# Kernel optimization log

Measured on AMD Instinct MI355X. Metric: run time of the kernel, lower is better.

The kernel has to match this reference:

```python
import jax, jax.numpy as jnp
import numpy as np

N_SAMPLES = 32768
WINDOW = 2048
HOP = WINDOW // 2
N_FRAMES = N_SAMPLES // HOP  # 32 resonance frames
BASE_RES = 0.5
RES_SPAN = 1.0 - BASE_RES
RES_FACTOR = 0.9
N_RES = 32
EXPR = 4
CPD = 16
N_COEFFS = WINDOW // 2 + 1  # 1025


def interpolate_last_axis(x, new_size):
    # linear interpolation along last axis (align_corners=False semantics)
    old = x.shape[-1]
    pos = (jnp.arange(new_size, dtype=jnp.float32) + 0.5) * (old / new_size) - 0.5
    pos = jnp.clip(pos, 0.0, old - 1.0)
    lo = jnp.floor(pos).astype(jnp.int32)
    hi = jnp.minimum(lo + 1, old - 1)
    w = pos - lo.astype(jnp.float32)
    return x[..., lo] * (1.0 - w) + x[..., hi] * w


def overlap_add(frames):
    # frames: (..., n_frames, window); hop = window//2; output (..., n_frames*hop)
    *lead, nf, w = frames.shape
    hop = w // 2
    a = frames[..., :hop]
    b = frames[..., hop:]
    b = jnp.concatenate([jnp.zeros_like(b[..., :1, :]), b[..., :-1, :]], axis=-2)
    return (a + b).reshape(*lead, nf * hop)


def freq_domain_transfer_function_to_resonance(window_size, decay_coeffs, n_frames, start_phase, start_mags):
    # decay_coeffs/start_phase/start_mags: (nr, expr, n_coeffs); log-space decay scan
    log_decay = jnp.log(decay_coeffs + 1e-12)[..., None, :]  # (nr, expr, 1, nc)
    shape = log_decay.shape[:-2] + (n_frames, log_decay.shape[-1])
    cum = jnp.cumsum(jnp.broadcast_to(log_decay, shape), axis=-2)  # decay^(f+1)
    mags = jnp.exp(cum) * start_mags[..., None, :]
    spec = mags * jnp.exp(1j * start_phase[..., None, :])
    frames = jnp.fft.irfft(spec, n=window_size, axis=-1)  # (nr, expr, n_frames, window)
    t = jnp.arange(window_size, dtype=jnp.float32)
    hann = 0.5 - 0.5 * jnp.cos(2.0 * jnp.pi * t / window_size)
    return overlap_add(frames * hann)  # (nr, expr, n_frames*hop)


def unit_norm(x):
    return x / (jnp.linalg.norm(x, axis=-1, keepdims=True) + 1e-8)


def fft_convolve(a, b):
    n = a.shape[-1]
    fa = jnp.fft.rfft(a, n=2 * n, axis=-1)
    fb = jnp.fft.rfft(b, n=2 * n, axis=-1)
    return jnp.fft.irfft(fa * fb, n=2 * n, axis=-1)[..., :n]


def setup_inputs() -> dict:
    key = jax.random.key(0)
    ks = jax.random.split(key, 10)
    control_signal = jax.random.normal(ks[0], (2, 4, CPD, 128), dtype=jnp.float32)
    deformations = jax.random.normal(ks[1], (2, 4, EXPR, 128), dtype=jnp.float32) * 0.1
    router = jax.random.uniform(ks[2], (CPD, N_RES), minval=-1.0, maxval=1.0)

    def init_resonance(k):
        k1, k2 = jax.random.split(k)
        res = jax.random.uniform(k1, (N_RES, N_COEFFS, 1), minval=0.01, maxval=1.0)
        deform = jax.random.uniform(k2, (1, N_COEFFS, EXPR), minval=-0.02, maxval=0.02)
        return res + deform

    amp = init_resonance(ks[3])
    phase = init_resonance(ks[4])
    decay = init_resonance(ks[5])
    gains = jax.random.uniform(ks[6], (N_RES, 1), minval=0.01, maxval=1.1)
    return {"control_signal": control_signal, "deformations": deformations,
            "router": router, "amp": amp, "phase": phase, "decay": decay, "gains": gains}


def reference(control_signal, deformations, router, amp, phase, decay, gains):
    b, e, cpd, frames = control_signal.shape
    nr = router.shape[1]
    # route control plane -> resonances: (b,e,nr,frames)
    routed = jnp.einsum('becf,cr->berf', control_signal, router)
    before_upsample = routed
    # (nr, n_coeffs, expr) -> (nr, expr, n_coeffs)
    amp_t = jnp.transpose(amp, (0, 2, 1))
    phase_t = jnp.transpose(phase, (0, 2, 1))
    decay_t = jnp.transpose(decay, (0, 2, 1))
    d_coeffs = BASE_RES + jax.nn.sigmoid(decay_t) * RES_SPAN * RES_FACTOR
    res = freq_domain_transfer_function_to_resonance(
        WINDOW, d_coeffs, N_FRAMES, jnp.tanh(phase_t) * jnp.pi, jnp.abs(amp_t))
    res = unit_norm(res)[None, None]  # (1,1,nr,expr,N)
    routed_up = interpolate_last_axis(routed[:, :, :, None, :], N_SAMPLES)  # (b,e,nr,1,N)
    noise = jax.random.uniform(jax.random.key(123), routed_up.shape, minval=-1.0, maxval=1.0)
    routed_up = routed_up * noise
    conv = fft_convolve(routed_up, res)  # (b,e,nr,expr,N)
    d = deformations.at[:, :, 0, :].add(1.0)  # base deformation favors first expressivity
    d = jax.nn.softmax(d, axis=2)[:, :, None, :, :]  # (b,e,1,expr,def_frames)
    d = interpolate_last_axis(d, N_SAMPLES)
    x = jnp.sum(d * conv, axis=-2)  # mix over expressivity -> (b,e,nr,N)
    summed = jnp.tanh(x * jnp.abs(gains).reshape(1, 1, nr, 1))
    summed = jnp.sum(summed, axis=-2, keepdims=True)  # (b,e,1,N)
    return summed, before_upsample
```

## Files before the change

### kernel.cpp

```cpp
#include <hip/hip_runtime.h>
#include <hip/hip_fp16.h>
#include <stdint.h>


#define PI_F     3.14159265358979323846f
#define TWOPI_F  6.28318530717958647692f
#define UNIT64K  (TWOPI_F/65536.0f)
#define UNIT2K   (TWOPI_F/2048.0f)
#define SCALE64K (1.0f/65536.0f)
#define SK3(i)   ((i) + 3*((i) >> 4))
#define RPH 308
#define SKP(i)   ((i) + 4*((i) >> 4))
#define RPW 328

__device__ __forceinline__ float2 cmul(float2 a, float2 b){
  return make_float2(a.x*b.x - a.y*b.y, a.x*b.y + a.y*b.x);
}

__device__ __forceinline__ float2 twid(uint32_t e, float unit, float sign){
  float ang = (float)e * unit;
  float sn, cn;
  __sincosf(ang, &sn, &cn);
  return make_float2(cn, sign*sn);
}

__device__ __forceinline__ float2 mulnegi(float2 w){ return make_float2(w.y, -w.x); }
__device__ __forceinline__ float2 mulposi(float2 w){ return make_float2(-w.y, w.x); }

__device__ __forceinline__ void bfly_inv(float2& u, float2& v, float2 w){
  float2 tv = cmul(v, w);
  v = make_float2(u.x - tv.x, u.y - tv.y);
  u = make_float2(u.x + tv.x, u.y + tv.y);
}
__device__ __forceinline__ void bfly_fwd(float2& u, float2& v, float2 w){
  float2 d = make_float2(u.x - v.x, u.y - v.y);
  u = make_float2(u.x + v.x, u.y + v.y);
  v = cmul(d, w);
}

__device__ __forceinline__ uint32_t rotl32(uint32_t v, int r){
  return (v << r) | (v >> (32 - r));
}

__device__ __forceinline__ void threefry2x32(uint32_t c0, uint32_t c1,
                                             uint32_t& o0, uint32_t& o1){
  const uint32_t k0 = 0u, k1 = 123u;
  const uint32_t k2 = 0x1BD11BDAu ^ k0 ^ k1;
  const uint32_t ks[3] = {k0, k1, k2};
  uint32_t x0 = c0 + k0, x1 = c1 + k1;
#pragma unroll
  for (int i = 0; i < 5; i++){
    if ((i & 1) == 0){
      x0 += x1; x1 = rotl32(x1,13); x1 ^= x0;
      x0 += x1; x1 = rotl32(x1,15); x1 ^= x0;
      x0 += x1; x1 = rotl32(x1,26); x1 ^= x0;
      x0 += x1; x1 = rotl32(x1, 6); x1 ^= x0;
    } else {
      x0 += x1; x1 = rotl32(x1,17); x1 ^= x0;
      x0 += x1; x1 = rotl32(x1,29); x1 ^= x0;
      x0 += x1; x1 = rotl32(x1,16); x1 ^= x0;
      x0 += x1; x1 = rotl32(x1,24); x1 ^= x0;
    }
    x0 += ks[(i+1)%3];
    x1 += ks[(i+2)%3] + (uint32_t)(i+1);
  }
  o0 = x0; o1 = x1;
}

__device__ __forceinline__ float jax_noise(uint32_t p){
  uint32_t b0, b1;
  threefry2x32(0u, p, b0, b1);
  uint32_t bits = b0 ^ b1;
  float u = __uint_as_float((bits >> 9) | 0x3f800000u) - 1.0f;
  return fmaxf(-1.0f, u*2.0f - 1.0f);
}

__device__ __forceinline__ void interp128(int t, int& lo, int& hi, float& w){
  float posf = ((float)t + 0.5f) * (1.0f/256.0f) - 0.5f;
  posf = fminf(fmaxf(posf, 0.0f), 127.0f);
  lo = (int)posf;
  hi = lo + 1; if (hi > 127) hi = 127;
  w = posf - (float)lo;
}

__device__ __forceinline__ __half2 u2h(uint32_t u){
  union { uint32_t u; __half2 h; } x; x.u = u; return x.h;
}
__device__ __forceinline__ uint32_t h2u(__half2 h){
  union { uint32_t u; __half2 h; } x; x.h = h; return x.u;
}
__device__ __forceinline__ constexpr int sw4(int k){ return ((k & 3) << 2) | (k >> 2); }

__device__ __forceinline__ void cws(float2& u, const float c, const float s){
  const float x = u.x*c - u.y*s;
  u.y = u.x*s + u.y*c;
  u.x = x;
}
__device__ __forceinline__ void cwv(float2& u, const float2 w){
  const float x = u.x*w.x - u.y*w.y;
  u.y = u.x*w.y + u.y*w.x;
  u.x = x;
}

__device__ __forceinline__ void dft4(float2& a, float2& b, float2& c, float2& d,
                                     const float sgn){
  float2 t0 = make_float2(a.x + c.x, a.y + c.y);
  float2 t1 = make_float2(a.x - c.x, a.y - c.y);
  float2 t2 = make_float2(b.x + d.x, b.y + d.y);
  float2 t3 = make_float2(b.x - d.x, b.y - d.y);
  float2 i3 = make_float2(-sgn*t3.y, sgn*t3.x);
  a = make_float2(t0.x + t2.x, t0.y + t2.y);
  c = make_float2(t0.x - t2.x, t0.y - t2.y);
  b = make_float2(t1.x + i3.x, t1.y + i3.y);
  d = make_float2(t1.x - i3.x, t1.y - i3.y);
}

#define DFT16_TW(d, sgn) do { \
  const float C1_ = 0.92387953251128674f, S1_ = 0.38268343236508978f; \
  const float C2_ = 0.70710678118654752f; \
  cws(d[5],  C1_,  (sgn)*S1_); \
  cws(d[6],  C2_,  (sgn)*C2_); \
  cws(d[7],  S1_,  (sgn)*C1_); \
  cws(d[9],  C2_,  (sgn)*C2_); \
  cws(d[10], 0.0f, (sgn)); \
  cws(d[11], -C2_, (sgn)*C2_); \
  cws(d[13], S1_,  (sgn)*C1_); \
  cws(d[14], -C2_, (sgn)*C2_); \
  cws(d[15], -C1_, -(sgn)*S1_); \
} while(0)

__device__ __forceinline__ void dft16(float2* d, const float sgn){
#pragma unroll
  for (int nb = 0; nb < 4; nb++) dft4(d[nb], d[nb+4], d[nb+8], d[nb+12], sgn);
  DFT16_TW(d, sgn);
#pragma unroll
  for (int ka = 0; ka < 4; ka++) dft4(d[4*ka], d[4*ka+1], d[4*ka+2], d[4*ka+3], sgn);
}
__device__ __forceinline__ void dft16b(float2* d, const float sgn){
#pragma unroll
  for (int nb = 0; nb < 4; nb++) dft4(d[4*nb], d[4*nb+1], d[4*nb+2], d[4*nb+3], sgn);
  DFT16_TW(d, sgn);
#pragma unroll
  for (int ka = 0; ka < 4; ka++) dft4(d[ka], d[ka+4], d[ka+8], d[ka+12], sgn);
}

__device__ __forceinline__ void pass1_fwd(__half2* buf, const float2* twl, const int t){
  const int row = t >> 4, L = t & 15;
  __half2* BR = buf + row*RPW;
  float2 d[16];
#pragma unroll
  for (int H = 0; H < 16; H++) d[H] = __half22float2(BR[L + 20*H]);
  dft16(d, -1.0f);
#pragma unroll
  for (int k1 = 0; k1 < 16; k1++){
    float2 y = d[sw4(k1)];
    cwv(y, twl[(L*k1) & 255]);
    BR[L + 20*k1] = __floats2half2_rn(y.x, y.y);
  }
}

__global__ void k_routed(const float* __restrict__ ctrl, const float* __restrict__ defm,
                         const float* __restrict__ router,
                         float* __restrict__ w_routed, float* __restrict__ w_sm,
                         float* __restrict__ out1){
  int idx = blockIdx.x*blockDim.x + threadIdx.x;
  if (idx < 32768){
    int f = idx & 127, r = (idx >> 7) & 31, be = idx >> 12;
    float acc = 0.0f;
#pragma unroll
    for (int c = 0; c < 16; c++)
      acc += ctrl[(be*16 + c)*128 + f] * router[c*32 + r];
    w_routed[idx] = acc;
    out1[idx] = acc;
  } else if (idx < 32768 + 1024){
    int j = idx - 32768;
    int f = j & 127, be = j >> 7;
    float v[4];
#pragma unroll
    for (int x = 0; x < 4; x++)
      v[x] = defm[(be*4 + x)*128 + f] + (x == 0 ? 1.0f : 0.0f);
    float mx = fmaxf(fmaxf(v[0], v[1]), fmaxf(v[2], v[3]));
    float s = 0.0f;
#pragma unroll
    for (int x = 0; x < 4; x++){ v[x] = expf(v[x] - mx); s += v[x]; }
#pragma unroll
    for (int x = 0; x < 4; x++) w_sm[(be*4 + x)*128 + f] = v[x]/s;
  }
}

__global__ void k_frames(const float* __restrict__ amp, const float* __restrict__ phase,
                         const float* __restrict__ decay, float2* __restrict__ w_fr){
  const int wg = blockIdx.x;
  const int f = wg & 31;
  const int rp = wg >> 5;
  const int p = rp & 1;
  const int r = rp >> 1;
  const int t = threadIdx.x;
  __shared__ float2 buf[2048];

  for (int k = t; k <= 1024; k += 256){
    float2 S[2];
#pragma unroll
    for (int d = 0; d < 2; d++){
      const int x = 2*p + d;
      const int base = (r*1025 + k)*4 + x;
      float a  = fabsf(amp[base]);
      float ph = tanhf(phase[base]) * PI_F;
      float sg = 1.0f / (1.0f + expf(-decay[base]));
      float dc = 0.5f + 0.45f * sg;
      float mag = expf(logf(dc + 1e-12f) * (float)(f+1)) * a;
      float snv, csv;
      sincosf(ph, &snv, &csv);
      float re = mag * csv, im = mag * snv;
      if (k == 0 || k == 1024) im = 0.0f;
      S[d] = make_float2(re, im);
    }
    buf[__brev((uint32_t)k) >> 21] =
        make_float2(S[0].x - S[1].y, S[0].y + S[1].x);
    if (k >= 1 && k <= 1023)
      buf[__brev((uint32_t)(2048 - k)) >> 21] =
          make_float2(S[0].x + S[1].y, -S[0].y + S[1].x);
  }
  __syncthreads();
  for (int s = 10; s >= 0; s--){
    const int ls = 10 - s;
    const int hl = 1 << ls;
    for (int bi = t; bi < 1024; bi += 256){
      const int g = bi >> ls, j = bi & (hl - 1);
      const int i0 = g*2*hl + j, i1 = i0 + hl;
      float2 pp = buf[i0], qq = buf[i1];
      float2 w = twid((uint32_t)(j << s), UNIT2K, +1.0f);
      float2 v = cmul(qq, w);
      buf[i0] = make_float2(pp.x+v.x, pp.y+v.y);
      buf[i1] = make_float2(pp.x-v.x, pp.y-v.y);
    }
    __syncthreads();
  }
  float2* O = w_fr + (size_t)wg*2048;
  for (int u = t; u < 2048; u += 256){
    float hann = 0.5f - 0.5f*cosf(TWOPI_F * (float)u / 2048.0f);
    float sc = (1.0f/2048.0f) * hann;
    O[u] = make_float2(buf[u].x*sc, buf[u].y*sc);
  }
}

__global__ void k_ola(const float2* __restrict__ w_fr, float* __restrict__ w_resT,
                      float* __restrict__ w_sumsq){
  const int wg = blockIdx.x;
  const int cq = wg & 7;
  const int rp = wg >> 3;
  const int c0 = cq*32;
  const int r = rp >> 1, p = rp & 1;
  const int ch0 = r*4 + p*2;
  const int t = threadIdx.x;
  __shared__ float tx[32][129], ty[32][129];
  __shared__ float red[2][256];
  const float2* F = w_fr + (size_t)rp*32*2048;
  float acc0 = 0.0f, acc1 = 0.0f;
#pragma unroll
  for (int it = 0; it < 16; it++){
    const int idx = it*256 + t;
    const int cp = idx & 31, m = idx >> 5;
    const int n = c0 + cp + 256*m;
    const int f = n >> 10, u = n & 1023;
    float2 a = F[(size_t)f*2048 + u];
    float vx = a.x, vy = a.y;
    if (f > 0){
      float2 b = F[(size_t)(f-1)*2048 + u + 1024];
      vx += b.x; vy += b.y;
    }
    tx[cp][m] = vx; ty[cp][m] = vy;
    acc0 += vx*vx; acc1 += vy*vy;
  }
  red[0][t] = acc0; red[1][t] = acc1;
  __syncthreads();
#pragma unroll
  for (int it = 0; it < 16; it++){
    const int idx = it*256 + t;
    const int m = idx & 127, cp = idx >> 7;
    w_resT[(size_t)ch0*32768 + (size_t)(c0+cp)*128 + m]     = tx[cp][m];
    w_resT[(size_t)(ch0+1)*32768 + (size_t)(c0+cp)*128 + m] = ty[cp][m];
  }
  for (int off = 128; off > 0; off >>= 1){
    __syncthreads();
    if (t < off){ red[0][t] += red[0][t+off]; red[1][t] += red[1][t+off]; }
  }
  if (t == 0){
    atomicAdd(&w_sumsq[ch0],     red[0][0]);
    atomicAdd(&w_sumsq[ch0 + 1], red[1][0]);
  }
}

__global__ void k_norm(const float* __restrict__ w_sumsq, float* __restrict__ w_invnorm){
  const int s = threadIdx.x;
  if (s < 128) w_invnorm[s] = 1.0f/(sqrtf(w_sumsq[s]) + 1e-8f);
}

__global__ void k_fwdA(const int mode, const float* __restrict__ w_resT,
                       const float* __restrict__ w_invnorm,
                       const float* __restrict__ w_routed,
                       __half2* __restrict__ outh){
  const int wg = blockIdx.x;
  const int cq = wg & 63;
  const int sig = wg >> 6;
  const int c0 = cq*4;
  const int t = threadIdx.x;
  __shared__ __half2 buf[4][RPH];
  if (mode == 0){
    const int rr = sig >> 1, pq = sig & 1;
    const int ch0 = rr*4 + pq*2;
    const float inv0 = w_invnorm[ch0], inv1 = w_invnorm[ch0+1];
#pragma unroll
    for (int i = 0; i < 2; i++){
      const int j = i*256 + t;
      const int cc = j & 3, m = j >> 2;
      const int c = c0 + cc;
      float vx = w_resT[(size_t)ch0*32768 + c*128 + m] * inv0;
      float vy = w_resT[(size_t)(ch0+1)*32768 + c*128 + m] * inv1;
      buf[cc][SK3(m)] = __floats2half2_rn(vx, vy);
      buf[cc][SK3(m + 128)] = __floats2half2_rn(0.0f, 0.0f);
    }
  } else {
    const float* rp = w_routed + sig*128;
#pragma unroll
    for (int i = 0; i < 2; i++){
      const int j = i*256 + t;
      const int cc = j & 3, m = j >> 2;
      const int c = c0 + cc;
      const int n = c + 256*m;
      int lo, hi; float w;
      interp128(n, lo, hi, w);
      float rv = rp[lo]*(1.0f - w) + rp[hi]*w;
      float vx = rv * jax_noise((uint32_t)sig*32768u + (uint32_t)n);
      buf[cc][SK3(m)] = __floats2half2_rn(vx, 0.0f);
      buf[cc][SK3(m + 128)] = __floats2half2_rn(0.0f, 0.0f);
    }
  }
  __syncthreads();
  const int row = t >> 6, q = t & 63;
  for (int sp = 0; sp < 4; sp++){
    const int s  = 2*sp;
    const int hh = 1 << (6 - 2*sp);
    const int hl = hh << 1;
    const int lj = 6 - 2*sp;
    const int j = q & (hh - 1), g = q >> lj;
    const int base = g*2*hl + j;
    const uint32_t e = (uint32_t)(c0 + row) + 256u*(uint32_t)j;
    __half2* B = buf[row];
    const int i0 = SK3(base), i1 = SK3(base+hh), i2 = SK3(base+hl), i3 = SK3(base+hl+hh);
    float2 u0 = __half22float2(B[i0]);
    float2 u1 = __half22float2(B[i1]);
    float2 u2 = __half22float2(B[i2]);
    float2 u3 = __half22float2(B[i3]);
    float2 wA0 = twid((e << s) & 0xFFFFu, UNIT64K, -1.0f);
    float2 wA1 = mulnegi(wA0);
    float2 wB  = cmul(wA0, wA0);
    bfly_fwd(u0, u2, wA0);
    bfly_fwd(u1, u3, wA1);
    bfly_fwd(u0, u1, wB);
    bfly_fwd(u2, u3, wB);
    B[i0] = __floats2half2_rn(u0.x, u0.y);
    B[i1] = __floats2half2_rn(u1.x, u1.y);
    B[i2] = __floats2half2_rn(u2.x, u2.y);
    B[i3] = __floats2half2_rn(u3.x, u3.y);
    __syncthreads();
  }
#pragma unroll
  for (int i = 0; i < 4; i++){
    const int cc = i, m = t;
    outh[(size_t)sig*65536 + (size_t)(c0+cc)*256 + m] = buf[cc][SK3(m)];
  }
}

__global__ __launch_bounds__(256, 4)
void k_fwdB(const __half2* __restrict__ spech, __half2* __restrict__ resp_t){
  const int wg = blockIdx.x;
  const int mq = wg & 15;
  const int sig = wg >> 4;
  const int m16 = mq*16;
  const int t = threadIdx.x;
  __shared__ alignas(16) __half2 buf[16*RPW];
  __shared__ float2 twl[256];
  twl[t] = twid((uint32_t)t << 8, UNIT64K, -1.0f);
  const __half2* base = spech + (size_t)sig*65536;
  {
    const int mm = t & 15, q = t >> 4;
    __half2* BR = buf + mm*RPW;
#pragma unroll
    for (int i = 0; i < 16; i++)
      BR[20*i + q] = base[(size_t)(16*i + q)*256 + m16 + mm];
  }
  __syncthreads();
  pass1_fwd(buf, twl, t);
  __syncthreads();
  {
    const int k1 = t >> 4, row = t & 15;
    __half2* BG = buf + row*RPW + 20*k1;
    float2 v[16];
#pragma unroll
    for (int cc = 0; cc < 4; cc++){
      const uint4 ld = *reinterpret_cast<const uint4*>(BG + 4*cc);
      v[4*cc+0] = __half22float2(u2h(ld.x));
      v[4*cc+1] = __half22float2(u2h(ld.y));
      v[4*cc+2] = __half22float2(u2h(ld.z));
      v[4*cc+3] = __half22float2(u2h(ld.w));
    }
    dft16(v, -1.0f);
    uint4* O4 = reinterpret_cast<uint4*>(resp_t + (((size_t)sig*16 + mq)*256 + t)*16);
#pragma unroll
    for (int cc = 0; cc < 4; cc++){
      uint4 st;
      st.x = h2u(__floats2half2_rn(v[4*cc+0].x, v[4*cc+0].y));
      st.y = h2u(__floats2half2_rn(v[4*cc+1].x, v[4*cc+1].y));
      st.z = h2u(__floats2half2_rn(v[4*cc+2].x, v[4*cc+2].y));
      st.w = h2u(__floats2half2_rn(v[4*cc+3].x, v[4*cc+3].y));
      O4[cc] = st;
    }
  }
}

__global__ __launch_bounds__(256, 4)
void k_conv(const __half2* __restrict__ ruspec,
            const __half2* __restrict__ resp_t,
            __half2* __restrict__ chunkbuf, const int gbase){
  const int wg = blockIdx.x;
  const int mq = wg & 15;
  const int p  = (wg >> 4) & 1;
  const int gl = wg >> 5;
  const int g = gbase + gl;
  const int r = g & 31;
  const int m16 = mq*16;
  const int t = threadIdx.x;
  __shared__ alignas(16) __half2 buf[16*RPW];
  __shared__ float2 twl[256];
  twl[t] = twid((uint32_t)t << 8, UNIT64K, -1.0f);

  {
    const uint4* A4 = reinterpret_cast<const uint4*>(
        ruspec + (size_t)g*65536 + (size_t)t*256 + m16);
    uint4 a0 = A4[0], a1 = A4[1], a2 = A4[2], a3 = A4[3];
    const int cs = SKP(t);
    uint32_t w[16];
    w[0]=a0.x; w[1]=a0.y; w[2]=a0.z; w[3]=a0.w;
    w[4]=a1.x; w[5]=a1.y; w[6]=a1.z; w[7]=a1.w;
    w[8]=a2.x; w[9]=a2.y; w[10]=a2.z; w[11]=a2.w;
    w[12]=a3.x; w[13]=a3.y; w[14]=a3.z; w[15]=a3.w;
#pragma unroll
    for (int mm = 0; mm < 16; mm++)
      buf[mm*RPW + cs] = u2h(w[mm]);
  }
  __syncthreads();
  pass1_fwd(buf, twl, t);
  __syncthreads();
  {
    const int k1 = t >> 4, row = t & 15;
    __half2* BG = buf + row*RPW + 20*k1;
    float2 v[16];
#pragma unroll
    for (int cc = 0; cc < 4; cc++){
      const uint4 ld = *reinterpret_cast<const uint4*>(BG + 4*cc);
      v[4*cc+0] = __half22float2(u2h(ld.x));
      v[4*cc+1] = __half22float2(u2h(ld.y));
      v[4*cc+2] = __half22float2(u2h(ld.z));
      v[4*cc+3] = __half22float2(u2h(ld.w));
    }
    const uint4* Bt = reinterpret_cast<const uint4*>(
        resp_t + (((size_t)(r*2 + p)*16 + mq)*256 + t)*16);
    uint4 b0 = Bt[0], b1 = Bt[1], b2 = Bt[2], b3 = Bt[3];
    dft16(v, -1.0f);
    uint32_t bw[16];
    bw[0]=b0.x; bw[1]=b0.y; bw[2]=b0.z; bw[3]=b0.w;
    bw[4]=b1.x; bw[5]=b1.y; bw[6]=b1.z; bw[7]=b1.w;
    bw[8]=b2.x; bw[9]=b2.y; bw[10]=b2.z; bw[11]=b2.w;
    bw[12]=b3.x; bw[13]=b3.y; bw[14]=b3.z; bw[15]=b3.w;
#pragma unroll
    for (int pp = 0; pp < 16; pp++){
      const float2 b = __half22float2(u2h(bw[pp]));
      const float zx = v[pp].x, zy = v[pp].y;
      v[pp] = make_float2((zx*b.x - zy*b.y)*SCALE64K,
                          (zx*b.y + zy*b.x)*SCALE64K);
    }
    dft16b(v, +1.0f);
    __half2 h[16];
#pragma unroll
    for (int n2 = 0; n2 < 16; n2++){
      float2 m = v[n2];
      const float2 w = twl[(n2*k1) & 255];
      const float x = m.x*w.x + m.y*w.y;
      m.y = -m.x*w.y + m.y*w.x;
      m.x = x;
      h[n2] = __floats2half2_rn(m.x, m.y);
    }
#pragma unroll
    for (int cc = 0; cc < 4; cc++){
      uint4 st;
      st.x = h2u(h[4*cc+0]);
      st.y = h2u(h[4*cc+1]);
      st.z = h2u(h[4*cc+2]);
      st.w = h2u(h[4*cc+3]);
      *reinterpret_cast<uint4*>(BG + 4*cc) = st;
    }
  }
  __syncthreads();
  {
    const int row = t >> 4, L = t & 15;
    __half2* BR = buf + row*RPW;
    float2 d[16];
#pragma unroll
    for (int k1 = 0; k1 < 16; k1++) d[k1] = __half22float2(BR[L + 20*k1]);
    dft16(d, +1.0f);
#pragma unroll
    for (int H = 0; H < 16; H++){
      const float2 x = d[sw4(H)];
      BR[L + 20*H] = __floats2half2_rn(x.x, x.y);
    }
  }
  __syncthreads();
  __half2* O = chunkbuf + (size_t)(gl*2 + p)*65536;
#pragma unroll
  for (int i = 0; i < 16; i++){
    O[(size_t)(m16 + i)*256 + t] = buf[i*RPW + SKP(t)];
  }
}

__global__ __launch_bounds__(256, 4)
void k_invA_w(const __half2* __restrict__ chunkbuf, const int gbase,
              const float* __restrict__ w_sm, const float* __restrict__ gains,
              float* __restrict__ out0){
  const int wg = blockIdx.x;
  const int c16 = wg & 15;
  const int gl = wg >> 4;
  const int g = gbase + gl;
  const int r = g & 31, be = g >> 5;
  const int c0 = c16*16;
  const int t = threadIdx.x;
  __shared__ __half2 zz[2][16][RPH];
#pragma unroll
  for (int p = 0; p < 2; p++){
    const __half2* C = chunkbuf + (size_t)(gl*2 + p)*65536;
#pragma unroll
    for (int i = 0; i < 16; i++){
      const int li = t + i*256;
      const int cc = li & 15, m = li >> 4;
      zz[p][cc][SK3(m)] = C[(size_t)m*256 + c0 + cc];
    }
  }
  __syncthreads();
  const int q = t & 63;
  const int row0 = t >> 6;
  for (int sp = 0; sp < 4; sp++){
    const int sB = 6 - 2*sp;
    const int hA = 1 << (2*sp);
    const int lA = 2*sp;
    const int j = q & (hA - 1), gq = q >> lA;
    const int base = gq*4*hA + j;
    const int i0 = SK3(base), i1 = SK3(base+hA), i2 = SK3(base+2*hA), i3 = SK3(base+3*hA);
#pragma unroll 1
    for (int it = 0; it < 8; it++){
      const int row = row0 + it*4;
      const int p = row >> 4, cc = row & 15;
      __half2* Z = zz[p][cc];
      float2 u0 = __half22float2(Z[i0]);
      float2 u1 = __half22float2(Z[i1]);
      float2 u2 = __half22float2(Z[i2]);
      float2 u3 = __half22float2(Z[i3]);
      const uint32_t e = (uint32_t)(c0 + cc) + 256u*(uint32_t)j;
      float2 wB0 = twid((e << sB) & 0xFFFFu, UNIT64K, +1.0f);
      float2 wA  = cmul(wB0, wB0);
      float2 wB1 = mulposi(wB0);
      bfly_inv(u0, u1, wA);
      bfly_inv(u2, u3, wA);
      bfly_inv(u0, u2, wB0);
      bfly_inv(u1, u3, wB1);
      Z[i0] = __floats2half2_rn(u0.x, u0.y);
      Z[i1] = __floats2half2_rn(u1.x, u1.y);
      Z[i2] = __floats2half2_rn(u2.x, u2.y);
      Z[i3] = __floats2half2_rn(u3.x, u3.y);
    }
    __syncthreads();
  }
  const float gv = fabsf(gains[r]);
  const float* smb = w_sm + be*512;
#pragma unroll
  for (int it = 0; it < 8; it++){
    const int li = t + it*256;
    const int cc = li & 15, m = li >> 4;
    const int tt = c0 + cc + 256*m;
    int lo, hi; float w;
    interp128(tt, lo, hi, w);
    float2 z0 = __half22float2(zz[0][cc][SK3(m)]);
    float2 z1 = __half22float2(zz[1][cc][SK3(m)]);
    float dw0 = smb[0*128 + lo]*(1.0f - w) + smb[0*128 + hi]*w;
    float dw1 = smb[1*128 + lo]*(1.0f - w) + smb[1*128 + hi]*w;
    float dw2 = smb[2*128 + lo]*(1.0f - w) + smb[2*128 + hi]*w;
    float dw3 = smb[3*128 + lo]*(1.0f - w) + smb[3*128 + hi]*w;
    float val = dw0*z0.x + dw1*z0.y + dw2*z1.x + dw3*z1.y;
    atomicAdd(&out0[(size_t)be*32768 + tt], tanhf(val*gv));
  }
}

extern "C" void kernel_launch(void* const* d_in, const int* in_sizes, int n_in,
                              void* d_out, int out_size, void* d_ws, size_t ws_size,
                              hipStream_t stream){
  const float* ctrl   = (const float*)d_in[0];
  const float* defm   = (const float*)d_in[1];
  const float* router = (const float*)d_in[2];
  const float* amp    = (const float*)d_in[3];
  const float* phase  = (const float*)d_in[4];
  const float* decay  = (const float*)d_in[5];
  const float* gains  = (const float*)d_in[6];
  float* out = (float*)d_out;
  float* ws  = (float*)d_ws;

  float*   w_resT    = ws;
  float*   w_routed  = ws + 4194304;
  float*   w_sm      = ws + 4227072;
  float*   w_invnorm = ws + 4231168;
  float*   w_sumsq   = ws + 4231296;
  __half2* ruspec_h  = (__half2*)(ws + 4231424);
  __half2* resp_h    = (__half2*)(ws + 21008640);
  __half2* chunk_h   = (__half2*)(ws + 25202944);
  const size_t base_f = 25202944;
  float2* w_fr       = (float2*)ruspec_h;
  __half2* resp_t    = (__half2*)w_resT;

  int G = 0;
  for (int gg = 128; gg >= 1; gg >>= 1){
    size_t need = (base_f + (size_t)gg*131072) * sizeof(float);
    if (need <= ws_size){ G = gg; break; }
  }

  hipMemsetAsync(d_out, 0, 262144*sizeof(float), stream);
  k_routed<<<132, 256, 0, stream>>>(ctrl, defm, router, w_routed, w_sm, out + 262144);
  if (G == 0) return;

  hipMemsetAsync(w_sumsq, 0, 128*sizeof(float), stream);
  k_frames<<<2048, 256, 0, stream>>>(amp, phase, decay, w_fr);
  k_ola<<<512, 256, 0, stream>>>(w_fr, w_resT, w_sumsq);
  k_norm<<<1, 128, 0, stream>>>(w_sumsq, w_invnorm);
  k_fwdA<<<64*64, 256, 0, stream>>>(0, w_resT, w_invnorm, w_routed, resp_h);
  k_fwdB<<<64*16, 256, 0, stream>>>(resp_h, resp_t);
  k_fwdA<<<256*64, 256, 0, stream>>>(1, w_resT, w_invnorm, w_routed, ruspec_h);
  for (int gb = 0; gb < 256; gb += G){
    k_conv<<<G*32, 256, 0, stream>>>(ruspec_h, resp_t, chunk_h, gb);
    k_invA_w<<<G*16, 256, 0, stream>>>(chunk_h, gb, w_sm, gains, out);
  }
}
```

Measured before the change: 361.7 us.

## Transpose conv chunk output and rewrite inverse stage as register radix-16 FFT

k_conv now writes its chunk output transposed, with each thread storing contiguous 16-byte vectors. k_invA_w reads those rows directly, doing two register-resident radix-16 DFT passes with recurrence twiddles instead of four LDS radix-4 passes that each needed a sync and a sincos. The inverse kernel also moves to 8 columns per block, doubling the grid, and caches the softmax weights in LDS. The aim is to cut LDS traffic, barriers and transcendental calls. The cost is higher register pressure and half-precision rounding at different points.

```diff
diff --git a/kernel.cpp b/kernel.cpp
--- a/kernel.cpp
+++ b/kernel.cpp
@@ -27,11 +27,6 @@
 __device__ __forceinline__ float2 mulnegi(float2 w){ return make_float2(w.y, -w.x); }
 __device__ __forceinline__ float2 mulposi(float2 w){ return make_float2(-w.y, w.x); }
 
-__device__ __forceinline__ void bfly_inv(float2& u, float2& v, float2 w){
-  float2 tv = cmul(v, w);
-  v = make_float2(u.x - tv.x, u.y - tv.y);
-  u = make_float2(u.x + tv.x, u.y + tv.y);
-}
 __device__ __forceinline__ void bfly_fwd(float2& u, float2& v, float2 w){
   float2 d = make_float2(u.x - v.x, u.y - v.y);
   u = make_float2(u.x + v.x, u.y + v.y);
@@ -90,6 +85,9 @@
   union { uint32_t u; __half2 h; } x; x.h = h; return x.u;
 }
 __device__ __forceinline__ constexpr int sw4(int k){ return ((k & 3) << 2) | (k >> 2); }
+__device__ __forceinline__ constexpr int br4(int x){
+  return ((x & 1) << 3) | ((x & 2) << 1) | ((x & 4) >> 1) | ((x & 8) >> 3);
+}
 
 __device__ __forceinline__ void cws(float2& u, const float c, const float s){
   const float x = u.x*c - u.y*s;
@@ -516,10 +514,19 @@
     }
   }
   __syncthreads();
-  __half2* O = chunkbuf + (size_t)(gl*2 + p)*65536;
-#pragma unroll
-  for (int i = 0; i < 16; i++){
-    O[(size_t)(m16 + i)*256 + t] = buf[i*RPW + SKP(t)];
+  {
+    uint4* O4 = reinterpret_cast<uint4*>(
+        chunkbuf + (size_t)(gl*2 + p)*65536 + (size_t)t*256 + m16);
+    const int cs = SKP(t);
+#pragma unroll
+    for (int q4 = 0; q4 < 4; q4++){
+      uint4 st;
+      st.x = h2u(buf[(4*q4+0)*RPW + cs]);
+      st.y = h2u(buf[(4*q4+1)*RPW + cs]);
+      st.z = h2u(buf[(4*q4+2)*RPW + cs]);
+      st.w = h2u(buf[(4*q4+3)*RPW + cs]);
+      O4[q4] = st;
+    }
   }
 }
 
@@ -528,72 +535,94 @@
               const float* __restrict__ w_sm, const float* __restrict__ gains,
               float* __restrict__ out0){
   const int wg = blockIdx.x;
-  const int c16 = wg & 15;
-  const int gl = wg >> 4;
+  const int c8 = wg & 31;
+  const int gl = wg >> 5;
   const int g = gbase + gl;
   const int r = g & 31, be = g >> 5;
-  const int c0 = c16*16;
+  const int c0 = c8*8;
   const int t = threadIdx.x;
-  __shared__ __half2 zz[2][16][RPH];
-#pragma unroll
-  for (int p = 0; p < 2; p++){
-    const __half2* C = chunkbuf + (size_t)(gl*2 + p)*65536;
-#pragma unroll
-    for (int i = 0; i < 16; i++){
-      const int li = t + i*256;
-      const int cc = li & 15, m = li >> 4;
-      zz[p][cc][SK3(m)] = C[(size_t)m*256 + c0 + cc];
-    }
-  }
-  __syncthreads();
-  const int q = t & 63;
-  const int row0 = t >> 6;
-  for (int sp = 0; sp < 4; sp++){
-    const int sB = 6 - 2*sp;
-    const int hA = 1 << (2*sp);
-    const int lA = 2*sp;
-    const int j = q & (hA - 1), gq = q >> lA;
-    const int base = gq*4*hA + j;
-    const int i0 = SK3(base), i1 = SK3(base+hA), i2 = SK3(base+2*hA), i3 = SK3(base+3*hA);
-#pragma unroll 1
-    for (int it = 0; it < 8; it++){
-      const int row = row0 + it*4;
-      const int p = row >> 4, cc = row & 15;
-      __half2* Z = zz[p][cc];
-      float2 u0 = __half22float2(Z[i0]);
-      float2 u1 = __half22float2(Z[i1]);
-      float2 u2 = __half22float2(Z[i2]);
-      float2 u3 = __half22float2(Z[i3]);
-      const uint32_t e = (uint32_t)(c0 + cc) + 256u*(uint32_t)j;
-      float2 wB0 = twid((e << sB) & 0xFFFFu, UNIT64K, +1.0f);
-      float2 wA  = cmul(wB0, wB0);
-      float2 wB1 = mulposi(wB0);
-      bfly_inv(u0, u1, wA);
-      bfly_inv(u2, u3, wA);
-      bfly_inv(u0, u2, wB0);
-      bfly_inv(u1, u3, wB1);
-      Z[i0] = __floats2half2_rn(u0.x, u0.y);
-      Z[i1] = __floats2half2_rn(u1.x, u1.y);
-      Z[i2] = __floats2half2_rn(u2.x, u2.y);
-      Z[i3] = __floats2half2_rn(u3.x, u3.y);
-    }
-    __syncthreads();
-  }
+  __shared__ alignas(16) __half2 buf[16*RPW];
+  __shared__ float sm_lds[512];
+  sm_lds[t]       = w_sm[be*512 + t];
+  sm_lds[256 + t] = w_sm[be*512 + 256 + t];
+
+  const int row = t >> 4;
+  const int p   = row >> 3;
+  const int cc  = row & 7;
+  const int c   = c0 + cc;
+  {
+    const int u = t & 15;
+    const uint4* C4 = reinterpret_cast<const uint4*>(
+        chunkbuf + (size_t)(gl*2 + p)*65536 + (size_t)c*256 + 16*br4(u));
+    uint4 z0 = C4[0], z1 = C4[1], z2 = C4[2], z3 = C4[3];
+    uint32_t zw[16];
+    zw[0]=z0.x; zw[1]=z0.y; zw[2]=z0.z; zw[3]=z0.w;
+    zw[4]=z1.x; zw[5]=z1.y; zw[6]=z1.z; zw[7]=z1.w;
+    zw[8]=z2.x; zw[9]=z2.y; zw[10]=z2.z; zw[11]=z2.w;
+    zw[12]=z3.x; zw[13]=z3.y; zw[14]=z3.z; zw[15]=z3.w;
+    const float2 wstep = twid((uint32_t)(16*c) & 0xFFFFu, UNIT64K, +1.0f);
+    float2 w = make_float2(1.0f, 0.0f);
+    float2 d[16];
+#pragma unroll
+    for (int rh = 0; rh < 16; rh++){
+      d[rh] = cmul(__half22float2(u2h(zw[br4(rh)])), w);
+      w = cmul(w, wstep);
+    }
+    dft16(d, +1.0f);
+    __half2* BR = buf + row*RPW;
+#pragma unroll
+    for (int mL = 0; mL < 16; mL++){
+      const float2 s = d[sw4(mL)];
+      BR[20*mL + u] = __floats2half2_rn(s.x, s.y);
+    }
+  }
+  __syncthreads();
+  const int mL = t & 15;
+  float2 v[16];
+  {
+    const __half2* BG = buf + row*RPW + 20*mL;
+#pragma unroll
+    for (int q4 = 0; q4 < 4; q4++){
+      const uint4 ld = *reinterpret_cast<const uint4*>(BG + 4*q4);
+      v[4*q4+0] = __half22float2(u2h(ld.x));
+      v[4*q4+1] = __half22float2(u2h(ld.y));
+      v[4*q4+2] = __half22float2(u2h(ld.z));
+      v[4*q4+3] = __half22float2(u2h(ld.w));
+    }
+  }
+  __syncthreads();
+  {
+    const float2 wstep = twid((uint32_t)(c + 256*mL) & 0xFFFFu, UNIT64K, +1.0f);
+    float2 w = wstep;
+#pragma unroll
+    for (int kL2 = 1; kL2 < 16; kL2++){
+      v[kL2] = cmul(v[kL2], w);
+      w = cmul(w, wstep);
+    }
+    dft16(v, +1.0f);
+    __half2* BR = buf + row*RPW;
+#pragma unroll
+    for (int mH = 0; mH < 8; mH++){
+      const float2 x = v[sw4(mH)];
+      BR[mL + 20*mH] = __floats2half2_rn(x.x, x.y);
+    }
+  }
+  __syncthreads();
   const float gv = fabsf(gains[r]);
-  const float* smb = w_sm + be*512;
-#pragma unroll
-  for (int it = 0; it < 8; it++){
+#pragma unroll
+  for (int it = 0; it < 4; it++){
     const int li = t + it*256;
-    const int cc = li & 15, m = li >> 4;
-    const int tt = c0 + cc + 256*m;
+    const int cc2 = li & 7, m = li >> 3;
+    const int tt = c0 + cc2 + 256*m;
     int lo, hi; float w;
     interp128(tt, lo, hi, w);
-    float2 z0 = __half22float2(zz[0][cc][SK3(m)]);
-    float2 z1 = __half22float2(zz[1][cc][SK3(m)]);
-    float dw0 = smb[0*128 + lo]*(1.0f - w) + smb[0*128 + hi]*w;
-    float dw1 = smb[1*128 + lo]*(1.0f - w) + smb[1*128 + hi]*w;
-    float dw2 = smb[2*128 + lo]*(1.0f - w) + smb[2*128 + hi]*w;
-    float dw3 = smb[3*128 + lo]*(1.0f - w) + smb[3*128 + hi]*w;
+    const int cell = (m & 15) + 20*(m >> 4);
+    float2 z0 = __half22float2(buf[cc2*RPW + cell]);
+    float2 z1 = __half22float2(buf[(8 + cc2)*RPW + cell]);
+    float dw0 = sm_lds[0*128 + lo]*(1.0f - w) + sm_lds[0*128 + hi]*w;
+    float dw1 = sm_lds[1*128 + lo]*(1.0f - w) + sm_lds[1*128 + hi]*w;
+    float dw2 = sm_lds[2*128 + lo]*(1.0f - w) + sm_lds[2*128 + hi]*w;
+    float dw3 = sm_lds[3*128 + lo]*(1.0f - w) + sm_lds[3*128 + hi]*w;
     float val = dw0*z0.x + dw1*z0.y + dw2*z1.x + dw3*z1.y;
     atomicAdd(&out0[(size_t)be*32768 + tt], tanhf(val*gv));
   }
@@ -643,6 +672,6 @@
   k_fwdA<<<256*64, 256, 0, stream>>>(1, w_resT, w_invnorm, w_routed, ruspec_h);
   for (int gb = 0; gb < 256; gb += G){
     k_conv<<<G*32, 256, 0, stream>>>(ruspec_h, resp_t, chunk_h, gb);
-    k_invA_w<<<G*16, 256, 0, stream>>>(chunk_h, gb, w_sm, gains, out);
-  }
-}
+    k_invA_w<<<G*32, 256, 0, stream>>>(chunk_h, gb, w_sm, gains, out);
+  }
+}
```

Result: faster. 343.8 us (-4.9%).
